# Kernel tuning notes

Hardware: AMD Instinct MI355X
Metric: run time of the kernel (lower is better)

Reference implementation:

```python
import jax, jax.numpy as jnp
import numpy as np

B, F, N, L, K = 16, 256, 16384, 4096, 9  # batch, channels, input pixels, pooled pixels, kernel


def setup_inputs() -> dict:
    key = jax.random.key(0)
    k1, k2 = jax.random.split(key, 2)
    input_images = jax.random.normal(k1, (B, F, N), dtype=jnp.float32)
    # raw indices in [-1, N-1]; -1 marks a missing neighbor (zero padding)
    raw = jax.random.randint(k2, (L, K), 0, N + 1) - 1
    mask = (raw != -1).astype(jnp.float32)          # prepare_mask: mask out -1 entries
    indices = jnp.maximum(raw, 0)                   # prepare_mask: clamp -1 -> 0
    return {"input_images": input_images, "indices": indices, "mask": mask}


def reference(input_images, indices, mask):
    # gather neighbor features: (B, F, L, K)
    col = input_images[..., indices] * mask
    # max over kernel (neighbor) axis -> pooled image (B, F, L)
    return jnp.max(col, axis=-1)
```

## Files before the change

kernel.cpp:

```cpp
#include <hip/hip_runtime.h>

#define B_ 16
#define F_ 256
#define N_ 16384
#define L_ 4096
#define K_ 9

__global__ __launch_bounds__(256) void prep_comb_kernel(
    const int* __restrict__ idx, const float* __restrict__ mask,
    unsigned short* __restrict__ comb) {
  int t = blockIdx.x * blockDim.x + threadIdx.x;
  if (t >= L_ * K_) return;
  int l = t / K_;
  int k = t - l * K_;
  int id = idx[t];
  float m = mask[t];
  comb[k * L_ + l] = (m != 0.0f) ? (unsigned short)id : (unsigned short)N_;
}

__global__ __launch_bounds__(256) void pool_kernel(
    const float* __restrict__ img, const unsigned short* __restrict__ comb,
    float* __restrict__ out) {
  __shared__ __align__(16) float row[N_ + 4];
  const int bf = blockIdx.x;
  const int tid = threadIdx.x;

  const float4* src4 = (const float4*)(img + (size_t)bf * N_);
  float4* row4 = (float4*)row;
#pragma unroll
  for (int i = 0; i < 16; ++i) {
    int j = i * 256 + tid;
    row4[j] = src4[j];
  }
  if (tid == 0) row[N_] = 0.0f;
  __syncthreads();

  float* outp = out + (size_t)bf * L_;
#pragma unroll
  for (int it = 0; it < L_ / 256; ++it) {
    int l = it * 256 + tid;
    float m = -INFINITY;
#pragma unroll
    for (int k = 0; k < K_; ++k) {
      int id = comb[k * L_ + l];
      m = fmaxf(m, row[id]);
    }
    outp[l] = m;
  }
}

__global__ __launch_bounds__(256) void pool_kernel_direct(
    const float* __restrict__ img, const int* __restrict__ idx,
    const float* __restrict__ mask, float* __restrict__ out) {
  __shared__ __align__(16) float row[N_ + 4];
  const int bf = blockIdx.x;
  const int tid = threadIdx.x;

  const float4* src4 = (const float4*)(img + (size_t)bf * N_);
  float4* row4 = (float4*)row;
#pragma unroll
  for (int i = 0; i < 16; ++i) {
    int j = i * 256 + tid;
    row4[j] = src4[j];
  }
  __syncthreads();

  float* outp = out + (size_t)bf * L_;
  for (int it = 0; it < L_ / 256; ++it) {
    int l = it * 256 + tid;
    float m = -INFINITY;
#pragma unroll
    for (int k = 0; k < K_; ++k) {
      int t = l * K_ + k;
      float v = (mask[t] != 0.0f) ? row[idx[t]] : 0.0f;
      m = fmaxf(m, v);
    }
    outp[l] = m;
  }
}

extern "C" void kernel_launch(void* const* d_in, const int* in_sizes, int n_in,
                              void* d_out, int out_size, void* d_ws, size_t ws_size,
                              hipStream_t stream) {
  const float* img = (const float*)d_in[0];
  const int* idx = (const int*)d_in[1];
  const float* mask = (const float*)d_in[2];
  float* out = (float*)d_out;

  const size_t comb_bytes = (size_t)L_ * K_ * sizeof(unsigned short);
  if (ws_size >= comb_bytes) {
    unsigned short* comb = (unsigned short*)d_ws;
    int total = L_ * K_;
    prep_comb_kernel<<<(total + 255) / 256, 256, 0, stream>>>(idx, mask, comb);
    pool_kernel<<<B_ * F_, 256, 0, stream>>>(img, comb, out);
  } else {
    pool_kernel_direct<<<B_ * F_, 256, 0, stream>>>(img, idx, mask, out);
  }
}
```

Before: 80.08 us.

## Pack per-pixel neighbor indices into 32-byte records and use 1024-thread blocks

The prep kernel now writes the 9 neighbor indices of each pooled pixel as one padded 16-entry ushort record, so the pool kernel reads them with two 16-byte vector loads instead of nine strided 2-byte loads. The pool kernel moves to 1024-thread blocks, so the row copy and the output loop each need fewer iterations per thread. The max is computed as a tree instead of a serial chain. The padded layout increases index traffic from 18 to 32 bytes per pixel, and larger blocks can lower occupancy given the 64 KB shared-memory row per block.

```diff
diff --git a/kernel.cpp b/kernel.cpp
--- a/kernel.cpp
+++ b/kernel.cpp
@@ -9,16 +9,26 @@
 __global__ __launch_bounds__(256) void prep_comb_kernel(
     const int* __restrict__ idx, const float* __restrict__ mask,
     unsigned short* __restrict__ comb) {
-  int t = blockIdx.x * blockDim.x + threadIdx.x;
-  if (t >= L_ * K_) return;
-  int l = t / K_;
-  int k = t - l * K_;
-  int id = idx[t];
-  float m = mask[t];
-  comb[k * L_ + l] = (m != 0.0f) ? (unsigned short)id : (unsigned short)N_;
+  int l = blockIdx.x * blockDim.x + threadIdx.x;
+  if (l >= L_) return;
+  unsigned short v[16];
+#pragma unroll
+  for (int k = 0; k < 16; ++k) v[k] = (unsigned short)N_;
+#pragma unroll
+  for (int k = 0; k < K_; ++k) {
+    int t = l * K_ + k;
+    int id = idx[t];
+    float m = mask[t];
+    v[k] = (m != 0.0f) ? (unsigned short)id : (unsigned short)N_;
+  }
+  uint4* dst = (uint4*)(comb) + (size_t)l * 2;
+  dst[0] = make_uint4(((unsigned)v[1] << 16) | v[0], ((unsigned)v[3] << 16) | v[2],
+                      ((unsigned)v[5] << 16) | v[4], ((unsigned)v[7] << 16) | v[6]);
+  dst[1] = make_uint4(((unsigned)v[9] << 16) | v[8], ((unsigned)v[11] << 16) | v[10],
+                      ((unsigned)v[13] << 16) | v[12], ((unsigned)v[15] << 16) | v[14]);
 }
 
-__global__ __launch_bounds__(256) void pool_kernel(
+__global__ __launch_bounds__(1024) void pool_kernel(
     const float* __restrict__ img, const unsigned short* __restrict__ comb,
     float* __restrict__ out) {
   __shared__ __align__(16) float row[N_ + 4];
@@ -28,8 +38,8 @@
   const float4* src4 = (const float4*)(img + (size_t)bf * N_);
   float4* row4 = (float4*)row;
 #pragma unroll
-  for (int i = 0; i < 16; ++i) {
-    int j = i * 256 + tid;
+  for (int i = 0; i < 4; ++i) {
+    int j = i * 1024 + tid;
     row4[j] = src4[j];
   }
   if (tid == 0) row[N_] = 0.0f;
@@ -37,15 +47,24 @@
 
   float* outp = out + (size_t)bf * L_;
 #pragma unroll
-  for (int it = 0; it < L_ / 256; ++it) {
-    int l = it * 256 + tid;
-    float m = -INFINITY;
-#pragma unroll
-    for (int k = 0; k < K_; ++k) {
-      int id = comb[k * L_ + l];
-      m = fmaxf(m, row[id]);
-    }
-    outp[l] = m;
+  for (int it = 0; it < L_ / 1024; ++it) {
+    int l = it * 1024 + tid;
+    const uint4* c = (const uint4*)(comb) + (size_t)l * 2;
+    uint4 a = c[0];
+    uint4 b = c[1];
+    float v0 = row[a.x & 0xffffu];
+    float v1 = row[a.x >> 16];
+    float v2 = row[a.y & 0xffffu];
+    float v3 = row[a.y >> 16];
+    float v4 = row[a.z & 0xffffu];
+    float v5 = row[a.z >> 16];
+    float v6 = row[a.w & 0xffffu];
+    float v7 = row[a.w >> 16];
+    float v8 = row[b.x & 0xffffu];
+    float t0 = fmaxf(fmaxf(v0, v1), v2);
+    float t1 = fmaxf(fmaxf(v3, v4), v5);
+    float t2 = fmaxf(fmaxf(v6, v7), v8);
+    outp[l] = fmaxf(fmaxf(t0, t1), t2);
   }
 }
 
@@ -87,12 +106,11 @@
   const float* mask = (const float*)d_in[2];
   float* out = (float*)d_out;
 
-  const size_t comb_bytes = (size_t)L_ * K_ * sizeof(unsigned short);
+  const size_t comb_bytes = (size_t)L_ * 16 * sizeof(unsigned short);
   if (ws_size >= comb_bytes) {
     unsigned short* comb = (unsigned short*)d_ws;
-    int total = L_ * K_;
-    prep_comb_kernel<<<(total + 255) / 256, 256, 0, stream>>>(idx, mask, comb);
-    pool_kernel<<<B_ * F_, 256, 0, stream>>>(img, comb, out);
+    prep_comb_kernel<<<(L_ + 255) / 256, 256, 0, stream>>>(idx, mask, comb);
+    pool_kernel<<<B_ * F_, 1024, 0, stream>>>(img, comb, out);
   } else {
     pool_kernel_direct<<<B_ * F_, 256, 0, stream>>>(img, idx, mask, out);
   }
```

Result: slower. 84.99 us (+6.1%).

## Persistent pair-interleaved pooling kernel with register-cached indices and prefetch

Applied to the files above, without the earlier changes.

Replaces the prep-plus-pool two-kernel scheme with one persistent kernel of 256 blocks of 1024 threads. Each block loops over 8 channel pairs. Two channel rows are interleaved into float2 in LDS so one gather serves both channels. The masked indices are packed once into registers per thread and reused across all pairs, and the next pair's rows are prefetched into registers while the current pair is computed. This aims to halve LDS gather instructions, remove the extra launch and the repeated index reads, and overlap global loads with compute. In exchange it uses 128KB of LDS per block and many registers, which limits occupancy, and adds block-wide barriers per pair.

```diff
diff --git a/kernel.cpp b/kernel.cpp
--- a/kernel.cpp
+++ b/kernel.cpp
@@ -6,76 +6,96 @@
 #define L_ 4096
 #define K_ 9
 
-__global__ __launch_bounds__(256) void prep_comb_kernel(
-    const int* __restrict__ idx, const float* __restrict__ mask,
-    unsigned short* __restrict__ comb) {
-  int t = blockIdx.x * blockDim.x + threadIdx.x;
-  if (t >= L_ * K_) return;
-  int l = t / K_;
-  int k = t - l * K_;
-  int id = idx[t];
-  float m = mask[t];
-  comb[k * L_ + l] = (m != 0.0f) ? (unsigned short)id : (unsigned short)N_;
-}
+#define NTHR 1024
+#define NBLK 256
+#define NPAIR (B_ * F_ / 2)
+#define PAIRS_PER_BLK (NPAIR / NBLK)
 
-__global__ __launch_bounds__(256) void pool_kernel(
-    const float* __restrict__ img, const unsigned short* __restrict__ comb,
-    float* __restrict__ out) {
-  __shared__ __align__(16) float row[N_ + 4];
-  const int bf = blockIdx.x;
-  const int tid = threadIdx.x;
-
-  const float4* src4 = (const float4*)(img + (size_t)bf * N_);
-  float4* row4 = (float4*)row;
-#pragma unroll
-  for (int i = 0; i < 16; ++i) {
-    int j = i * 256 + tid;
-    row4[j] = src4[j];
-  }
-  if (tid == 0) row[N_] = 0.0f;
-  __syncthreads();
-
-  float* outp = out + (size_t)bf * L_;
-#pragma unroll
-  for (int it = 0; it < L_ / 256; ++it) {
-    int l = it * 256 + tid;
-    float m = -INFINITY;
-#pragma unroll
-    for (int k = 0; k < K_; ++k) {
-      int id = comb[k * L_ + l];
-      m = fmaxf(m, row[id]);
-    }
-    outp[l] = m;
-  }
-}
-
-__global__ __launch_bounds__(256) void pool_kernel_direct(
+__global__ __launch_bounds__(NTHR, 4) void pool_pair_kernel(
     const float* __restrict__ img, const int* __restrict__ idx,
     const float* __restrict__ mask, float* __restrict__ out) {
-  __shared__ __align__(16) float row[N_ + 4];
-  const int bf = blockIdx.x;
+  __shared__ __align__(16) float2 pairbuf[N_ + 2];
   const int tid = threadIdx.x;
+  const int bid = blockIdx.x;
 
-  const float4* src4 = (const float4*)(img + (size_t)bf * N_);
-  float4* row4 = (float4*)row;
+  unsigned cpk[18];
 #pragma unroll
-  for (int i = 0; i < 16; ++i) {
-    int j = i * 256 + tid;
-    row4[j] = src4[j];
+  for (int j = 0; j < 18; ++j) {
+    const int s0 = 2 * j, s1 = 2 * j + 1;
+    const int it0 = s0 / K_, k0 = s0 % K_;
+    const int it1 = s1 / K_, k1 = s1 % K_;
+    int t0 = (it0 * NTHR + tid) * K_ + k0;
+    int t1 = (it1 * NTHR + tid) * K_ + k1;
+    unsigned id0 = (mask[t0] != 0.0f) ? (unsigned)idx[t0] : (unsigned)N_;
+    unsigned id1 = (mask[t1] != 0.0f) ? (unsigned)idx[t1] : (unsigned)N_;
+    cpk[j] = id0 | (id1 << 16);
+  }
+
+  const float2* imgf2 = (const float2*)img;
+  float2 sa[8], sb[8];
+
+  {
+    const int pid = bid * PAIRS_PER_BLK;
+    const float2* A = imgf2 + (size_t)(2 * pid) * (N_ / 2);
+    const float2* Bp = A + (N_ / 2);
+#pragma unroll
+    for (int i = 0; i < 8; ++i) {
+      sa[i] = A[tid + i * NTHR];
+      sb[i] = Bp[tid + i * NTHR];
+    }
+    if (tid == 0) pairbuf[N_] = make_float2(0.0f, 0.0f);
+#pragma unroll
+    for (int i = 0; i < 8; ++i) {
+      int e = tid + i * NTHR;
+      *(float4*)(&pairbuf[2 * e]) =
+          make_float4(sa[i].x, sb[i].x, sa[i].y, sb[i].y);
+    }
   }
   __syncthreads();
 
-  float* outp = out + (size_t)bf * L_;
-  for (int it = 0; it < L_ / 256; ++it) {
-    int l = it * 256 + tid;
-    float m = -INFINITY;
+#pragma unroll 1
+  for (int p = 0; p < PAIRS_PER_BLK; ++p) {
+    const int pid = bid * PAIRS_PER_BLK + p;
+
+    if (p + 1 < PAIRS_PER_BLK) {
+      const float2* A = imgf2 + (size_t)(2 * (pid + 1)) * (N_ / 2);
+      const float2* Bp = A + (N_ / 2);
 #pragma unroll
-    for (int k = 0; k < K_; ++k) {
-      int t = l * K_ + k;
-      float v = (mask[t] != 0.0f) ? row[idx[t]] : 0.0f;
-      m = fmaxf(m, v);
+      for (int i = 0; i < 8; ++i) {
+        sa[i] = A[tid + i * NTHR];
+        sb[i] = Bp[tid + i * NTHR];
+      }
     }
-    outp[l] = m;
+
+    float* outA = out + (size_t)(2 * pid) * L_;
+    float* outB = outA + L_;
+#pragma unroll
+    for (int it = 0; it < 4; ++it) {
+      int l = it * NTHR + tid;
+      float ma = -INFINITY, mb = -INFINITY;
+#pragma unroll
+      for (int k = 0; k < K_; ++k) {
+        const int slot = it * K_ + k;
+        unsigned w = cpk[slot >> 1];
+        unsigned id = (slot & 1) ? (w >> 16) : (w & 0xffffu);
+        float2 v = pairbuf[id];
+        ma = fmaxf(ma, v.x);
+        mb = fmaxf(mb, v.y);
+      }
+      outA[l] = ma;
+      outB[l] = mb;
+    }
+    __syncthreads();
+
+    if (p + 1 < PAIRS_PER_BLK) {
+#pragma unroll
+      for (int i = 0; i < 8; ++i) {
+        int e = tid + i * NTHR;
+        *(float4*)(&pairbuf[2 * e]) =
+            make_float4(sa[i].x, sb[i].x, sa[i].y, sb[i].y);
+      }
+      __syncthreads();
+    }
   }
 }
 
@@ -86,14 +106,5 @@
   const int* idx = (const int*)d_in[1];
   const float* mask = (const float*)d_in[2];
   float* out = (float*)d_out;
-
-  const size_t comb_bytes = (size_t)L_ * K_ * sizeof(unsigned short);
-  if (ws_size >= comb_bytes) {
-    unsigned short* comb = (unsigned short*)d_ws;
-    int total = L_ * K_;
-    prep_comb_kernel<<<(total + 255) / 256, 256, 0, stream>>>(idx, mask, comb);
-    pool_kernel<<<B_ * F_, 256, 0, stream>>>(img, comb, out);
-  } else {
-    pool_kernel_direct<<<B_ * F_, 256, 0, stream>>>(img, idx, mask, out);
-  }
+  pool_pair_kernel<<<NBLK, NTHR, 0, stream>>>(img, idx, mask, out);
 }
```

New measurement: 90.66 us. 13.2% more time.
